# Kernel optimization log

Hardware: AMD Instinct MI355X
Metric: run time of the kernel (lower is better)

## Reference

```python
import jax, jax.numpy as jnp
import numpy as np

K = 3          # kernel size (3x3 branch of SConv_2d)
STRIDE = 1
PAD = 1
NONCENTER = jnp.array([0, 1, 2, 3, 5, 6, 7, 8])      # drop center (idx 4) before sort
REORDER = jnp.array([0, 1, 2, 3, 8, 4, 5, 6, 7])     # reinsert center in the middle


def setup_inputs() -> dict:
    key = jax.random.key(0)
    k1, k2, k3, k4 = jax.random.split(key, 4)
    B, Cin, H, Wd = 8, 64, 128, 128
    Cout = 128
    x = jax.random.normal(k1, (B, Cin, H, Wd), dtype=jnp.float32)
    Coefficient = jax.random.normal(k2, (K * K, K * K), dtype=jnp.float32)
    W = jax.random.normal(k3, (Cout, Cin, K, K), dtype=jnp.float32) * 0.05
    b = jax.random.normal(k4, (Cout,), dtype=jnp.float32) * 0.05
    return {"x": x, "Coefficient": Coefficient, "W": W, "b": b}


def reference(x, Coefficient, W, b):
    # pad (same=False -> constant padding PAD on all sides)
    xp = jnp.pad(x, ((0, 0), (0, 0), (PAD, PAD), (PAD, PAD)))
    B, C, Hp, Wp = xp.shape
    Ho = (Hp - K) // STRIDE + 1
    Wo = (Wp - K) // STRIDE + 1
    # unfold: patches[b, kh*K+kw, c, h, w] == torch unfold+view+permute layout [B, KH*KW, C, H*W]
    patches = jnp.stack(
        [xp[:, :, i:i + Ho * STRIDE:STRIDE, j:j + Wo * STRIDE:STRIDE]
         for i in range(K) for j in range(K)], axis=1)           # [B, 9, C, Ho, Wo]
    center = patches[:, 4:5]                                      # [B, 1, C, Ho, Wo]
    y = jnp.einsum('bjchw,ij->bichw', patches, Coefficient)       # [B, 9, C, Ho, Wo]
    ys = jnp.sort(y[:, NONCENTER], axis=1)                        # sort 8 non-center taps
    z = jnp.concatenate([ys, center], axis=1)                     # [B, 9, C, Ho, Wo]
    z = z[:, REORDER]
    # view(B, KH, KW, C, H, W).permute(0,3,4,1,5,2) -> [B, C, KH*H, KW*W]
    z = z.reshape(B, K, K, C, Ho, Wo).transpose(0, 3, 4, 1, 5, 2).reshape(B, C, K * Ho, K * Wo)
    out = jax.lax.conv_general_dilated(
        z, W, window_strides=(K, K), padding='VALID',
        dimension_numbers=('NCHW', 'OIHW', 'NCHW'))
    return out + b[None, :, None, None]
```

## Files before the change

kernel.cpp:

```cpp
#include <hip/hip_runtime.h>
#include <hip/hip_bf16.h>


#define B_   8
#define C_   64
#define H_   128
#define W_   128
#define CO_  128
#define K_   576
#define MT   64
#define SROW 584

typedef __attribute__((ext_vector_type(8)))  short  short8;
typedef __attribute__((ext_vector_type(8)))  __bf16 bf16x8;
typedef __attribute__((ext_vector_type(16))) float  f32x16;
typedef __attribute__((ext_vector_type(2)))  float  f32x2;

__device__ __forceinline__ void cswap2(f32x2 &a, f32x2 &b) {
    f32x2 lo = __builtin_elementwise_min(a, b);
    f32x2 hi = __builtin_elementwise_max(a, b);
    a = lo; b = hi;
}

__device__ __forceinline__ ushort f2bf(float f) {
    union { float f; unsigned u; } v; v.f = f;
    unsigned r = v.u + 0x7fffu + ((v.u >> 16) & 1u);
    return (ushort)(r >> 16);
}

__device__ __forceinline__ unsigned pack2bf(float lo, float hi) {
    union { __hip_bfloat162 h; unsigned u; } cv;
    cv.h = __float22bfloat162_rn(make_float2(lo, hi));
    return cv.u;
}

__global__ __launch_bounds__(256) void conv_W_bf16(const float* __restrict__ Wg,
                                                   ushort* __restrict__ Wb) {
    int i = blockIdx.x * 256 + threadIdx.x;
    if (i >= CO_ * K_) return;
    const int e    = i & 7;
    const int lane = (i >> 3) & 63;
    const int t9   = i >> 9;
    const int nt   = t9 / 36;
    const int ks   = t9 - nt * 36;
    const int co   = nt * 32 + (lane & 31);
    const int kp   = ks * 16 + (lane >> 5) * 8 + e;
    int c, t;
    if (kp < 512) { const int rc = kp >> 3; t = kp & 7; c = ((rc & 7) << 3) | (rc >> 3); }
    else          { c = kp - 512; t = 8; }
    Wb[i] = f2bf(Wg[co * K_ + c * 9 + t]);
}

__global__ __launch_bounds__(512, 4) void sconv_mfma(
    const float* __restrict__ x,
    const float* __restrict__ Coef,
    const ushort* __restrict__ Wb,
    const float* __restrict__ bias,
    float* __restrict__ out)
{
    __shared__ __align__(16) ushort Zl[MT * SROW];

    const int tid = threadIdx.x;
    const int bx  = blockIdx.x;
    const int wq  = bx & 7;
    const int hq  = (bx >> 3) & 31;
    const int b   = bx >> 8;
    const int w0  = wq * 16;
    const int h0  = hq * 4;

    const int wave = tid >> 6;
    const int lane = tid & 63;
    const int mt   = wave >> 2;
    const int nt   = wave & 3;
    const int r31  = lane & 31;
    const int u    = lane >> 5;
    const ushort* bptr = Wb + ((size_t)(nt * 36) * 64 + lane) * 8;

    {
        const int j  = (tid >> 3) & 7;
        const int c  = wave + 8 * j;
        const int pw = tid & 7;
        const int w  = w0 + pw * 2;
        const float* xb = x + ((size_t)(b * C_ + c)) * (H_ * W_);

        float r[6][4];
        const bool interior = (h0 >= 4) && (h0 <= 120) && (w0 >= 16) && (w0 <= 96);
        if (interior) {
            const float* bp = xb + (h0 - 1) * W_ + (w - 1);
            #pragma unroll
            for (int dy = 0; dy < 6; ++dy) {
                float4 v; __builtin_memcpy(&v, bp + dy * W_, 16);
                r[dy][0] = v.x; r[dy][1] = v.y; r[dy][2] = v.z; r[dy][3] = v.w;
            }
        } else {
            const int wm = w - 1;
            const int wc = min(max(wm, 0), W_ - 4);
            const int s  = wm - wc;
            #pragma unroll
            for (int dy = 0; dy < 6; ++dy) {
                const int hy  = h0 + dy - 1;
                const bool hok = (unsigned)hy < (unsigned)H_;
                const int hc  = min(max(hy, 0), H_ - 1);
                float4 v; __builtin_memcpy(&v, xb + hc * W_ + wc, 16);
                const float rr0 = (s < 0) ? 0.f : ((s > 0) ? v.y : v.x);
                const float rr1 = (s < 0) ? v.x : ((s > 0) ? v.z : v.y);
                const float rr2 = (s < 0) ? v.y : ((s > 0) ? v.w : v.z);
                const float rr3 = (s < 0) ? v.z : ((s > 0) ? 0.f : v.w);
                r[dy][0] = hok ? rr0 : 0.f;
                r[dy][1] = hok ? rr1 : 0.f;
                r[dy][2] = hok ? rr2 : 0.f;
                r[dy][3] = hok ? rr3 : 0.f;
            }
        }

        const int rcb  = (wave * 8 + j) << 4;
        const int tailb = 1024 + 2 * c;
        #pragma unroll
        for (int hl = 0; hl < 4; ++hl) {
            f32x2 p2[9];
            #pragma unroll
            for (int dy = 0; dy < 3; ++dy)
                #pragma unroll
                for (int dx = 0; dx < 3; ++dx)
                    p2[dy * 3 + dx] = (f32x2){ r[hl + dy][dx], r[hl + dy][dx + 1] };

            f32x2 v2[8];
            #pragma unroll
            for (int ii = 0; ii < 8; ++ii) {
                const int i = ii + (ii >> 2);
                f32x2 acc = p2[0] * Coef[i * 9];
                #pragma unroll
                for (int jj = 1; jj < 9; ++jj) acc += p2[jj] * Coef[i * 9 + jj];
                v2[ii] = acc;
            }

            cswap2(v2[0],v2[1]); cswap2(v2[2],v2[3]); cswap2(v2[4],v2[5]); cswap2(v2[6],v2[7]);
            cswap2(v2[0],v2[2]); cswap2(v2[1],v2[3]); cswap2(v2[4],v2[6]); cswap2(v2[5],v2[7]);
            cswap2(v2[1],v2[2]); cswap2(v2[5],v2[6]);
            cswap2(v2[0],v2[4]); cswap2(v2[1],v2[5]); cswap2(v2[2],v2[6]); cswap2(v2[3],v2[7]);
            cswap2(v2[2],v2[4]); cswap2(v2[3],v2[5]);
            cswap2(v2[1],v2[2]); cswap2(v2[3],v2[4]); cswap2(v2[5],v2[6]);

            f32x2 z2[9] = { v2[0], v2[1], v2[2], v2[3], p2[4],
                            v2[4], v2[5], v2[6], v2[7] };

            char* zb0 = (char*)Zl + (size_t)(hl * 16 + pw * 2) * (SROW * 2);
            char* zb1 = zb0 + SROW * 2;
            uint4 q0 = make_uint4(pack2bf(z2[0][0], z2[1][0]), pack2bf(z2[2][0], z2[3][0]),
                                  pack2bf(z2[4][0], z2[5][0]), pack2bf(z2[6][0], z2[7][0]));
            uint4 q1 = make_uint4(pack2bf(z2[0][1], z2[1][1]), pack2bf(z2[2][1], z2[3][1]),
                                  pack2bf(z2[4][1], z2[5][1]), pack2bf(z2[6][1], z2[7][1]));
            *(uint4*)(zb0 + rcb) = q0;
            *(uint4*)(zb1 + rcb) = q1;
            *(ushort*)(zb0 + tailb) = f2bf(z2[8][0]);
            *(ushort*)(zb1 + tailb) = f2bf(z2[8][1]);
        }
    }

    short8 bq[8];
    #pragma unroll
    for (int i = 0; i < 8; ++i) bq[i] = *(const short8*)(bptr + i * 512);

    __syncthreads();

    const int arow = mt * 32 + r31;
    const char* abase = (const char*)Zl + (size_t)arow * (SROW * 2) + u * 16;

    bf16x8 aq[4];
    #pragma unroll
    for (int i = 0; i < 4; ++i)
        aq[i] = *(const bf16x8*)(abase + i * 32);

    f32x16 acc = {};

    #pragma unroll
    for (int ks = 0; ks < 36; ++ks) {
        bf16x8 a  = aq[ks & 3];
        short8 bb = bq[ks & 7];
        if (ks + 4 < 36)
            aq[ks & 3] = *(const bf16x8*)(abase + (ks + 4) * 32);
        if (ks + 8 < 36)
            bq[ks & 7] = *(const short8*)(bptr + (ks + 8) * 512);
        acc = __builtin_amdgcn_mfma_f32_32x32x16_bf16(a, __builtin_bit_cast(bf16x8, bb), acc, 0, 0, 0);
    }

    const int co = nt * 32 + r31;
    const float bv = bias[co];
    float* obase = out + (((size_t)(b * CO_ + co)) * H_ + h0 + mt * 2) * W_ + w0;
    #pragma unroll
    for (int qq = 0; qq < 4; ++qq) {
        const int roff = qq * 8 + u * 4;
        const int hl   = roff >> 4;
        const int wl   = roff & 15;
        float4 vv = make_float4(acc[qq*4+0] + bv, acc[qq*4+1] + bv,
                                acc[qq*4+2] + bv, acc[qq*4+3] + bv);
        *(float4*)(obase + hl * W_ + wl) = vv;
    }
}

#define WT 16
__device__ __forceinline__ void cswap(float &a, float &b) {
    float lo = fminf(a, b);
    float hi = fmaxf(a, b);
    a = lo; b = hi;
}
__global__ __launch_bounds__(256) void sconv_fp32(
    const float* __restrict__ x, const float* __restrict__ Coef,
    const float* __restrict__ Wg, const float* __restrict__ bias,
    float* __restrict__ out)
{
    __shared__ float Cf[81];
    __shared__ float Zl[C_ * 9 * WT];
    const int tid = threadIdx.x;
    const int bx  = blockIdx.x;
    const int wt  = bx & 7;
    const int h   = (bx >> 3) & 127;
    const int b   = bx >> 10;
    const int w0  = wt * WT;
    if (tid < 81) Cf[tid] = Coef[tid];
    __syncthreads();
    for (int task = tid; task < C_ * WT; task += 256) {
        const int c = task >> 4, wl = task & 15, w = w0 + wl;
        const float* xb = x + (b * C_ + c) * H_ * W_;
        float p[9];
        #pragma unroll
        for (int dy = 0; dy < 3; ++dy) {
            const int hy = h + dy - 1; const bool hin = (unsigned)hy < (unsigned)H_;
            #pragma unroll
            for (int dx = 0; dx < 3; ++dx) {
                const int wx = w + dx - 1; const bool win = (unsigned)wx < (unsigned)W_;
                p[dy * 3 + dx] = (hin && win) ? xb[hy * W_ + wx] : 0.0f;
            }
        }
        float v[8];
        #pragma unroll
        for (int ii = 0; ii < 8; ++ii) {
            const int i = ii + (ii >> 2);
            float acc = 0.0f;
            #pragma unroll
            for (int j = 0; j < 9; ++j) acc = fmaf(Cf[i * 9 + j], p[j], acc);
            v[ii] = acc;
        }
        cswap(v[0], v[1]); cswap(v[2], v[3]); cswap(v[4], v[5]); cswap(v[6], v[7]);
        cswap(v[0], v[2]); cswap(v[1], v[3]); cswap(v[4], v[6]); cswap(v[5], v[7]);
        cswap(v[1], v[2]); cswap(v[5], v[6]);
        cswap(v[0], v[4]); cswap(v[1], v[5]); cswap(v[2], v[6]); cswap(v[3], v[7]);
        cswap(v[2], v[4]); cswap(v[3], v[5]);
        cswap(v[1], v[2]); cswap(v[3], v[4]); cswap(v[5], v[6]);
        const int base = c * 9 * WT + wl;
        Zl[base + 0*WT]=v[0]; Zl[base + 1*WT]=v[1]; Zl[base + 2*WT]=v[2]; Zl[base + 3*WT]=v[3];
        Zl[base + 4*WT]=p[4];
        Zl[base + 5*WT]=v[4]; Zl[base + 6*WT]=v[5]; Zl[base + 7*WT]=v[6]; Zl[base + 8*WT]=v[7];
    }
    __syncthreads();
    const int co = tid >> 1, w0l = (tid & 1) * 8;
    float acc[8];
    #pragma unroll
    for (int i = 0; i < 8; ++i) acc[i] = 0.0f;
    for (int c = 0; c < C_; ++c) {
        #pragma unroll
        for (int t = 0; t < 9; ++t) {
            const float wv = Wg[(co * C_ + c) * 9 + t];
            const float* zp = &Zl[(c * 9 + t) * WT + w0l];
            const float4 za = *(const float4*)zp;
            const float4 zb = *(const float4*)(zp + 4);
            acc[0]=fmaf(za.x,wv,acc[0]); acc[1]=fmaf(za.y,wv,acc[1]);
            acc[2]=fmaf(za.z,wv,acc[2]); acc[3]=fmaf(za.w,wv,acc[3]);
            acc[4]=fmaf(zb.x,wv,acc[4]); acc[5]=fmaf(zb.y,wv,acc[5]);
            acc[6]=fmaf(zb.z,wv,acc[6]); acc[7]=fmaf(zb.w,wv,acc[7]);
        }
    }
    const float bv = bias[co];
    float* op = out + ((b * CO_ + co) * H_ + h) * W_ + w0 + w0l;
    *(float4*)(op)     = make_float4(acc[0]+bv, acc[1]+bv, acc[2]+bv, acc[3]+bv);
    *(float4*)(op + 4) = make_float4(acc[4]+bv, acc[5]+bv, acc[6]+bv, acc[7]+bv);
}

extern "C" void kernel_launch(void* const* d_in, const int* in_sizes, int n_in,
                              void* d_out, int out_size, void* d_ws, size_t ws_size,
                              hipStream_t stream) {
    const float* x    = (const float*)d_in[0];
    const float* Coef = (const float*)d_in[1];
    const float* Wg   = (const float*)d_in[2];
    const float* bias = (const float*)d_in[3];
    float* out = (float*)d_out;

    const size_t need = (size_t)CO_ * K_ * sizeof(ushort);
    if (ws_size >= need) {
        ushort* Wb = (ushort*)d_ws;
        conv_W_bf16<<<(CO_ * K_ + 255) / 256, 256, 0, stream>>>(Wg, Wb);
        sconv_mfma<<<B_ * (H_ / 4) * (W_ / 16), 512, 0, stream>>>(x, Coef, Wb, bias, out);
    } else {
        sconv_fp32<<<B_ * H_ * 8, 256, 0, stream>>>(x, Coef, Wg, bias, out);
    }
}
```

Before: 143.7 us.

## Halve spatial tile and split K across waves with LDS reduction

Each block now covers 2 output rows instead of 4, which doubles the grid and halves the LDS tile. The 8 waves split the 36-step K loop into two halves of 18 per N-tile. The two partial accumulators are combined through LDS before the bias add and store. This aims to raise occupancy (launch bounds 4 to 6 blocks) and shorten each wave's MFMA chain. In exchange, the halo reload overhead per output row doubles, two extra barriers and an LDS reduction are added, and the same weights are reloaded by twice as many blocks.

Measured after the change: 135.8 us. 1.06x faster.

```diff
diff --git a/kernel.cpp b/kernel.cpp
--- a/kernel.cpp
+++ b/kernel.cpp
@@ -8,7 +8,7 @@
 #define W_   128
 #define CO_  128
 #define K_   576
-#define MT   64
+#define MT   32
 #define SROW 584
 
 typedef __attribute__((ext_vector_type(8)))  short  short8;
@@ -51,7 +51,7 @@
     Wb[i] = f2bf(Wg[co * K_ + c * 9 + t]);
 }
 
-__global__ __launch_bounds__(512, 4) void sconv_mfma(
+__global__ __launch_bounds__(512, 6) void sconv_mfma(
     const float* __restrict__ x,
     const float* __restrict__ Coef,
     const ushort* __restrict__ Wb,
@@ -63,18 +63,18 @@
     const int tid = threadIdx.x;
     const int bx  = blockIdx.x;
     const int wq  = bx & 7;
-    const int hq  = (bx >> 3) & 31;
-    const int b   = bx >> 8;
+    const int hp  = (bx >> 3) & 63;
+    const int b   = bx >> 9;
     const int w0  = wq * 16;
-    const int h0  = hq * 4;
+    const int h0  = hp * 2;
 
     const int wave = tid >> 6;
     const int lane = tid & 63;
-    const int mt   = wave >> 2;
     const int nt   = wave & 3;
+    const int kh   = wave >> 2;
     const int r31  = lane & 31;
     const int u    = lane >> 5;
-    const ushort* bptr = Wb + ((size_t)(nt * 36) * 64 + lane) * 8;
+    const ushort* bptr = Wb + ((size_t)(nt * 36 + kh * 18) * 64 + lane) * 8;
 
     {
         const int j  = (tid >> 3) & 7;
@@ -83,12 +83,12 @@
         const int w  = w0 + pw * 2;
         const float* xb = x + ((size_t)(b * C_ + c)) * (H_ * W_);
 
-        float r[6][4];
-        const bool interior = (h0 >= 4) && (h0 <= 120) && (w0 >= 16) && (w0 <= 96);
+        float r[4][4];
+        const bool interior = (h0 >= 2) && (h0 <= 124) && (w0 >= 16) && (w0 <= 96);
         if (interior) {
             const float* bp = xb + (h0 - 1) * W_ + (w - 1);
             #pragma unroll
-            for (int dy = 0; dy < 6; ++dy) {
+            for (int dy = 0; dy < 4; ++dy) {
                 float4 v; __builtin_memcpy(&v, bp + dy * W_, 16);
                 r[dy][0] = v.x; r[dy][1] = v.y; r[dy][2] = v.z; r[dy][3] = v.w;
             }
@@ -97,7 +97,7 @@
             const int wc = min(max(wm, 0), W_ - 4);
             const int s  = wm - wc;
             #pragma unroll
-            for (int dy = 0; dy < 6; ++dy) {
+            for (int dy = 0; dy < 4; ++dy) {
                 const int hy  = h0 + dy - 1;
                 const bool hok = (unsigned)hy < (unsigned)H_;
                 const int hc  = min(max(hy, 0), H_ - 1);
@@ -116,7 +116,7 @@
         const int rcb  = (wave * 8 + j) << 4;
         const int tailb = 1024 + 2 * c;
         #pragma unroll
-        for (int hl = 0; hl < 4; ++hl) {
+        for (int hl = 0; hl < 2; ++hl) {
             f32x2 p2[9];
             #pragma unroll
             for (int dy = 0; dy < 3; ++dy)
@@ -157,44 +157,63 @@
         }
     }
 
-    short8 bq[8];
+    short8 bq[4];
     #pragma unroll
-    for (int i = 0; i < 8; ++i) bq[i] = *(const short8*)(bptr + i * 512);
-
-    __syncthreads();
-
-    const int arow = mt * 32 + r31;
-    const char* abase = (const char*)Zl + (size_t)arow * (SROW * 2) + u * 16;
-
-    bf16x8 aq[4];
+    for (int i = 0; i < 4; ++i) bq[i] = *(const short8*)(bptr + i * 512);
+
+    __syncthreads();
+
+    const char* abase = (const char*)Zl + (size_t)r31 * (SROW * 2) + u * 16
+                        + kh * 18 * 32;
+
+    bf16x8 aq[2];
+    aq[0] = *(const bf16x8*)(abase + 0);
+    aq[1] = *(const bf16x8*)(abase + 32);
+
+    f32x16 acc = {};
+
     #pragma unroll
-    for (int i = 0; i < 4; ++i)
-        aq[i] = *(const bf16x8*)(abase + i * 32);
-
-    f32x16 acc = {};
-
-    #pragma unroll
-    for (int ks = 0; ks < 36; ++ks) {
-        bf16x8 a  = aq[ks & 3];
-        short8 bb = bq[ks & 7];
-        if (ks + 4 < 36)
-            aq[ks & 3] = *(const bf16x8*)(abase + (ks + 4) * 32);
-        if (ks + 8 < 36)
-            bq[ks & 7] = *(const short8*)(bptr + (ks + 8) * 512);
+    for (int ksl = 0; ksl < 18; ++ksl) {
+        bf16x8 a  = aq[ksl & 1];
+        short8 bb = bq[ksl & 3];
+        if (ksl + 2 < 18)
+            aq[ksl & 1] = *(const bf16x8*)(abase + (ksl + 2) * 32);
+        if (ksl + 4 < 18)
+            bq[ksl & 3] = *(const short8*)(bptr + (ksl + 4) * 512);
         acc = __builtin_amdgcn_mfma_f32_32x32x16_bf16(a, __builtin_bit_cast(bf16x8, bb), acc, 0, 0, 0);
     }
 
-    const int co = nt * 32 + r31;
-    const float bv = bias[co];
-    float* obase = out + (((size_t)(b * CO_ + co)) * H_ + h0 + mt * 2) * W_ + w0;
-    #pragma unroll
-    for (int qq = 0; qq < 4; ++qq) {
-        const int roff = qq * 8 + u * 4;
-        const int hl   = roff >> 4;
-        const int wl   = roff & 15;
-        float4 vv = make_float4(acc[qq*4+0] + bv, acc[qq*4+1] + bv,
-                                acc[qq*4+2] + bv, acc[qq*4+3] + bv);
-        *(float4*)(obase + hl * W_ + wl) = vv;
+    __syncthreads();
+    float* scratch = (float*)Zl;
+    if (kh == 1) {
+        float* sp = scratch + nt * 1088 + lane * 17;
+        #pragma unroll
+        for (int qq = 0; qq < 4; ++qq)
+            *(float4*)(sp + qq * 4) = make_float4(acc[qq*4+0], acc[qq*4+1],
+                                                  acc[qq*4+2], acc[qq*4+3]);
+    }
+    __syncthreads();
+    if (kh == 0) {
+        const float* sp = scratch + nt * 1088 + lane * 17;
+        #pragma unroll
+        for (int qq = 0; qq < 4; ++qq) {
+            float4 pv = *(const float4*)(sp + qq * 4);
+            acc[qq*4+0] += pv.x; acc[qq*4+1] += pv.y;
+            acc[qq*4+2] += pv.z; acc[qq*4+3] += pv.w;
+        }
+
+        const int co = nt * 32 + r31;
+        const float bv = bias[co];
+        float* obase = out + (((size_t)(b * CO_ + co)) * H_ + h0) * W_ + w0;
+        #pragma unroll
+        for (int qq = 0; qq < 4; ++qq) {
+            const int roff = qq * 8 + u * 4;
+            const int hl   = roff >> 4;
+            const int wl   = roff & 15;
+            float4 vv = make_float4(acc[qq*4+0] + bv, acc[qq*4+1] + bv,
+                                    acc[qq*4+2] + bv, acc[qq*4+3] + bv);
+            *(float4*)(obase + hl * W_ + wl) = vv;
+        }
     }
 }
 
@@ -289,7 +308,7 @@
     if (ws_size >= need) {
         ushort* Wb = (ushort*)d_ws;
         conv_W_bf16<<<(CO_ * K_ + 255) / 256, 256, 0, stream>>>(Wg, Wb);
-        sconv_mfma<<<B_ * (H_ / 4) * (W_ / 16), 512, 0, stream>>>(x, Coef, Wb, bias, out);
+        sconv_mfma<<<B_ * (H_ / 2) * (W_ / 16), 512, 0, stream>>>(x, Coef, Wb, bias, out);
     } else {
         sconv_fp32<<<B_ * H_ * 8, 256, 0, stream>>>(x, Coef, Wg, bias, out);
     }
```

## Double-buffer Z tiles and loop four row-pair steps per block, overlapping transform with MFMA

Applied to the files above, without the earlier changes.

Each block now covers 8 output rows in four steps of 2 rows, using a double-buffered LDS Z tile so that waves 4-7 build the next tile's sorted-tap transform while waves 0-3 run the MFMA GEMM on the current one. Input rows are carried between steps so each step loads only 2 new rows, cutting the halo reloads. The grid is halved and only half the waves issue MFMAs. Per-block work becomes more serial, and waves 0-3 take part in both the transform and the MFMA phases.

Result: no change. 144.8 us (+0.8%).

```diff
diff --git a/kernel.cpp b/kernel.cpp
--- a/kernel.cpp
+++ b/kernel.cpp
@@ -8,8 +8,9 @@
 #define W_   128
 #define CO_  128
 #define K_   576
-#define MT   64
+#define MT   32
 #define SROW 584
+#define TB   4
 
 typedef __attribute__((ext_vector_type(8)))  short  short8;
 typedef __attribute__((ext_vector_type(8)))  __bf16 bf16x8;
@@ -51,6 +52,72 @@
     Wb[i] = f2bf(Wg[co * K_ + c * 9 + t]);
 }
 
+__device__ __forceinline__ void load_row(const float* __restrict__ xb, int hy,
+                                         int w, bool wint, float out[4]) {
+    if (wint && (unsigned)hy < (unsigned)H_) {
+        float4 v; __builtin_memcpy(&v, xb + hy * W_ + (w - 1), 16);
+        out[0] = v.x; out[1] = v.y; out[2] = v.z; out[3] = v.w;
+    } else {
+        const bool hok = (unsigned)hy < (unsigned)H_;
+        const int hc = min(max(hy, 0), H_ - 1);
+        const int wm = w - 1;
+        const int wc = min(max(wm, 0), W_ - 4);
+        const int s  = wm - wc;
+        float4 v; __builtin_memcpy(&v, xb + hc * W_ + wc, 16);
+        const float r0 = (s < 0) ? 0.f : ((s > 0) ? v.y : v.x);
+        const float r1 = (s < 0) ? v.x : ((s > 0) ? v.z : v.y);
+        const float r2 = (s < 0) ? v.y : ((s > 0) ? v.w : v.z);
+        const float r3 = (s < 0) ? v.z : ((s > 0) ? 0.f : v.w);
+        out[0] = hok ? r0 : 0.f; out[1] = hok ? r1 : 0.f;
+        out[2] = hok ? r2 : 0.f; out[3] = hok ? r3 : 0.f;
+    }
+}
+
+__device__ __forceinline__ void zstore_tile(const float (&rr)[4][4],
+                                            const float* __restrict__ Coef,
+                                            char* bufb, int rcb, int tailb, int pw) {
+    #pragma unroll
+    for (int hl = 0; hl < 2; ++hl) {
+        f32x2 p2[9];
+        #pragma unroll
+        for (int dy = 0; dy < 3; ++dy)
+            #pragma unroll
+            for (int dx = 0; dx < 3; ++dx)
+                p2[dy * 3 + dx] = (f32x2){ rr[hl + dy][dx], rr[hl + dy][dx + 1] };
+
+        f32x2 v2[8];
+        #pragma unroll
+        for (int ii = 0; ii < 8; ++ii) {
+            const int i = ii + (ii >> 2);
+            f32x2 acc = p2[0] * Coef[i * 9];
+            #pragma unroll
+            for (int jj = 1; jj < 9; ++jj) acc += p2[jj] * Coef[i * 9 + jj];
+            v2[ii] = acc;
+        }
+
+        cswap2(v2[0],v2[1]); cswap2(v2[2],v2[3]); cswap2(v2[4],v2[5]); cswap2(v2[6],v2[7]);
+        cswap2(v2[0],v2[2]); cswap2(v2[1],v2[3]); cswap2(v2[4],v2[6]); cswap2(v2[5],v2[7]);
+        cswap2(v2[1],v2[2]); cswap2(v2[5],v2[6]);
+        cswap2(v2[0],v2[4]); cswap2(v2[1],v2[5]); cswap2(v2[2],v2[6]); cswap2(v2[3],v2[7]);
+        cswap2(v2[2],v2[4]); cswap2(v2[3],v2[5]);
+        cswap2(v2[1],v2[2]); cswap2(v2[3],v2[4]); cswap2(v2[5],v2[6]);
+
+        f32x2 z2[9] = { v2[0], v2[1], v2[2], v2[3], p2[4],
+                        v2[4], v2[5], v2[6], v2[7] };
+
+        char* zb0 = bufb + (size_t)(hl * 16 + pw * 2) * (SROW * 2);
+        char* zb1 = zb0 + SROW * 2;
+        uint4 q0 = make_uint4(pack2bf(z2[0][0], z2[1][0]), pack2bf(z2[2][0], z2[3][0]),
+                              pack2bf(z2[4][0], z2[5][0]), pack2bf(z2[6][0], z2[7][0]));
+        uint4 q1 = make_uint4(pack2bf(z2[0][1], z2[1][1]), pack2bf(z2[2][1], z2[3][1]),
+                              pack2bf(z2[4][1], z2[5][1]), pack2bf(z2[6][1], z2[7][1]));
+        *(uint4*)(zb0 + rcb) = q0;
+        *(uint4*)(zb1 + rcb) = q1;
+        *(ushort*)(zb0 + tailb) = f2bf(z2[8][0]);
+        *(ushort*)(zb1 + tailb) = f2bf(z2[8][1]);
+    }
+}
+
 __global__ __launch_bounds__(512, 4) void sconv_mfma(
     const float* __restrict__ x,
     const float* __restrict__ Coef,
@@ -58,143 +125,90 @@
     const float* __restrict__ bias,
     float* __restrict__ out)
 {
-    __shared__ __align__(16) ushort Zl[MT * SROW];
+    __shared__ __align__(16) ushort Zl[2][MT * SROW];
 
     const int tid = threadIdx.x;
     const int bx  = blockIdx.x;
     const int wq  = bx & 7;
-    const int hq  = (bx >> 3) & 31;
-    const int b   = bx >> 8;
+    const int hq  = (bx >> 3) & 15;
+    const int b   = bx >> 7;
     const int w0  = wq * 16;
-    const int h0  = hq * 4;
+    const int h0b = hq * 8;
 
     const int wave = tid >> 6;
     const int lane = tid & 63;
-    const int mt   = wave >> 2;
     const int nt   = wave & 3;
     const int r31  = lane & 31;
     const int u    = lane >> 5;
     const ushort* bptr = Wb + ((size_t)(nt * 36) * 64 + lane) * 8;
 
-    {
-        const int j  = (tid >> 3) & 7;
-        const int c  = wave + 8 * j;
-        const int pw = tid & 7;
-        const int w  = w0 + pw * 2;
-        const float* xb = x + ((size_t)(b * C_ + c)) * (H_ * W_);
-
-        float r[6][4];
-        const bool interior = (h0 >= 4) && (h0 <= 120) && (w0 >= 16) && (w0 <= 96);
-        if (interior) {
-            const float* bp = xb + (h0 - 1) * W_ + (w - 1);
-            #pragma unroll
-            for (int dy = 0; dy < 6; ++dy) {
-                float4 v; __builtin_memcpy(&v, bp + dy * W_, 16);
-                r[dy][0] = v.x; r[dy][1] = v.y; r[dy][2] = v.z; r[dy][3] = v.w;
+    const int j  = (tid >> 3) & 7;
+    const int c  = wave + 8 * j;
+    const int pw = tid & 7;
+    const int w  = w0 + pw * 2;
+    const float* xb = x + ((size_t)(b * C_ + c)) * (H_ * W_);
+    const bool wint = (w0 >= 16) && (w0 <= 96);
+    const int rcb   = (wave * 8 + j) << 4;
+    const int tailb = 1024 + 2 * c;
+
+    short8 bq[4];
+    if (wave < 4) {
+        #pragma unroll
+        for (int i = 0; i < 4; ++i) bq[i] = *(const short8*)(bptr + i * 512);
+    }
+
+    float rr[4][4];
+    load_row(xb, h0b - 1, w, wint, rr[0]);
+    load_row(xb, h0b + 0, w, wint, rr[1]);
+    load_row(xb, h0b + 1, w, wint, rr[2]);
+    load_row(xb, h0b + 2, w, wint, rr[3]);
+    zstore_tile(rr, Coef, (char*)&Zl[0][0], rcb, tailb, pw);
+    __syncthreads();
+
+    for (int t = 0; t < TB; ++t) {
+        if (t < TB - 1) {
+            #pragma unroll
+            for (int q2 = 0; q2 < 4; ++q2) { rr[0][q2] = rr[2][q2]; rr[1][q2] = rr[3][q2]; }
+            const int h0n = h0b + 2 * (t + 1);
+            load_row(xb, h0n + 1, w, wint, rr[2]);
+            load_row(xb, h0n + 2, w, wint, rr[3]);
+            zstore_tile(rr, Coef, (char*)&Zl[(t + 1) & 1][0], rcb, tailb, pw);
+        }
+        if (wave < 4) {
+            const char* abase = (const char*)&Zl[t & 1][0] + (size_t)r31 * (SROW * 2) + u * 16;
+            bf16x8 aq[2];
+            aq[0] = *(const bf16x8*)(abase + 0);
+            aq[1] = *(const bf16x8*)(abase + 32);
+            f32x16 acc = {};
+            #pragma unroll
+            for (int ks = 0; ks < 36; ++ks) {
+                bf16x8 a  = aq[ks & 1];
+                short8 bb = bq[ks & 3];
+                if (ks + 2 < 36)
+                    aq[ks & 1] = *(const bf16x8*)(abase + (ks + 2) * 32);
+                if (ks + 4 < 36)
+                    bq[ks & 3] = *(const short8*)(bptr + (ks + 4) * 512);
+                acc = __builtin_amdgcn_mfma_f32_32x32x16_bf16(a, __builtin_bit_cast(bf16x8, bb), acc, 0, 0, 0);
             }
-        } else {
-            const int wm = w - 1;
-            const int wc = min(max(wm, 0), W_ - 4);
-            const int s  = wm - wc;
-            #pragma unroll
-            for (int dy = 0; dy < 6; ++dy) {
-                const int hy  = h0 + dy - 1;
-                const bool hok = (unsigned)hy < (unsigned)H_;
-                const int hc  = min(max(hy, 0), H_ - 1);
-                float4 v; __builtin_memcpy(&v, xb + hc * W_ + wc, 16);
-                const float rr0 = (s < 0) ? 0.f : ((s > 0) ? v.y : v.x);
-                const float rr1 = (s < 0) ? v.x : ((s > 0) ? v.z : v.y);
-                const float rr2 = (s < 0) ? v.y : ((s > 0) ? v.w : v.z);
-                const float rr3 = (s < 0) ? v.z : ((s > 0) ? 0.f : v.w);
-                r[dy][0] = hok ? rr0 : 0.f;
-                r[dy][1] = hok ? rr1 : 0.f;
-                r[dy][2] = hok ? rr2 : 0.f;
-                r[dy][3] = hok ? rr3 : 0.f;
+            if (t < TB - 1) {
+                #pragma unroll
+                for (int i = 0; i < 4; ++i) bq[i] = *(const short8*)(bptr + i * 512);
             }
-        }
-
-        const int rcb  = (wave * 8 + j) << 4;
-        const int tailb = 1024 + 2 * c;
-        #pragma unroll
-        for (int hl = 0; hl < 4; ++hl) {
-            f32x2 p2[9];
-            #pragma unroll
-            for (int dy = 0; dy < 3; ++dy)
-                #pragma unroll
-                for (int dx = 0; dx < 3; ++dx)
-                    p2[dy * 3 + dx] = (f32x2){ r[hl + dy][dx], r[hl + dy][dx + 1] };
-
-            f32x2 v2[8];
-            #pragma unroll
-            for (int ii = 0; ii < 8; ++ii) {
-                const int i = ii + (ii >> 2);
-                f32x2 acc = p2[0] * Coef[i * 9];
-                #pragma unroll
-                for (int jj = 1; jj < 9; ++jj) acc += p2[jj] * Coef[i * 9 + jj];
-                v2[ii] = acc;
+            const int h0t = h0b + 2 * t;
+            const int co  = nt * 32 + r31;
+            const float bv = bias[co];
+            float* obase = out + (((size_t)(b * CO_ + co)) * H_ + h0t) * W_ + w0;
+            #pragma unroll
+            for (int qq = 0; qq < 4; ++qq) {
+                const int roff = qq * 8 + u * 4;
+                const int hl   = roff >> 4;
+                const int wl   = roff & 15;
+                *(float4*)(obase + hl * W_ + wl) =
+                    make_float4(acc[qq*4+0] + bv, acc[qq*4+1] + bv,
+                                acc[qq*4+2] + bv, acc[qq*4+3] + bv);
             }
-
-            cswap2(v2[0],v2[1]); cswap2(v2[2],v2[3]); cswap2(v2[4],v2[5]); cswap2(v2[6],v2[7]);
-            cswap2(v2[0],v2[2]); cswap2(v2[1],v2[3]); cswap2(v2[4],v2[6]); cswap2(v2[5],v2[7]);
-            cswap2(v2[1],v2[2]); cswap2(v2[5],v2[6]);
-            cswap2(v2[0],v2[4]); cswap2(v2[1],v2[5]); cswap2(v2[2],v2[6]); cswap2(v2[3],v2[7]);
-            cswap2(v2[2],v2[4]); cswap2(v2[3],v2[5]);
-            cswap2(v2[1],v2[2]); cswap2(v2[3],v2[4]); cswap2(v2[5],v2[6]);
-
-            f32x2 z2[9] = { v2[0], v2[1], v2[2], v2[3], p2[4],
-                            v2[4], v2[5], v2[6], v2[7] };
-
-            char* zb0 = (char*)Zl + (size_t)(hl * 16 + pw * 2) * (SROW * 2);
-            char* zb1 = zb0 + SROW * 2;
-            uint4 q0 = make_uint4(pack2bf(z2[0][0], z2[1][0]), pack2bf(z2[2][0], z2[3][0]),
-                                  pack2bf(z2[4][0], z2[5][0]), pack2bf(z2[6][0], z2[7][0]));
-            uint4 q1 = make_uint4(pack2bf(z2[0][1], z2[1][1]), pack2bf(z2[2][1], z2[3][1]),
-                                  pack2bf(z2[4][1], z2[5][1]), pack2bf(z2[6][1], z2[7][1]));
-            *(uint4*)(zb0 + rcb) = q0;
-            *(uint4*)(zb1 + rcb) = q1;
-            *(ushort*)(zb0 + tailb) = f2bf(z2[8][0]);
-            *(ushort*)(zb1 + tailb) = f2bf(z2[8][1]);
-        }
-    }
-
-    short8 bq[8];
-    #pragma unroll
-    for (int i = 0; i < 8; ++i) bq[i] = *(const short8*)(bptr + i * 512);
-
-    __syncthreads();
-
-    const int arow = mt * 32 + r31;
-    const char* abase = (const char*)Zl + (size_t)arow * (SROW * 2) + u * 16;
-
-    bf16x8 aq[4];
-    #pragma unroll
-    for (int i = 0; i < 4; ++i)
-        aq[i] = *(const bf16x8*)(abase + i * 32);
-
-    f32x16 acc = {};
-
-    #pragma unroll
-    for (int ks = 0; ks < 36; ++ks) {
-        bf16x8 a  = aq[ks & 3];
-        short8 bb = bq[ks & 7];
-        if (ks + 4 < 36)
-            aq[ks & 3] = *(const bf16x8*)(abase + (ks + 4) * 32);
-        if (ks + 8 < 36)
-            bq[ks & 7] = *(const short8*)(bptr + (ks + 8) * 512);
-        acc = __builtin_amdgcn_mfma_f32_32x32x16_bf16(a, __builtin_bit_cast(bf16x8, bb), acc, 0, 0, 0);
-    }
-
-    const int co = nt * 32 + r31;
-    const float bv = bias[co];
-    float* obase = out + (((size_t)(b * CO_ + co)) * H_ + h0 + mt * 2) * W_ + w0;
-    #pragma unroll
-    for (int qq = 0; qq < 4; ++qq) {
-        const int roff = qq * 8 + u * 4;
-        const int hl   = roff >> 4;
-        const int wl   = roff & 15;
-        float4 vv = make_float4(acc[qq*4+0] + bv, acc[qq*4+1] + bv,
-                                acc[qq*4+2] + bv, acc[qq*4+3] + bv);
-        *(float4*)(obase + hl * W_ + wl) = vv;
+        }
+        __syncthreads();
     }
 }
 
@@ -238,7 +252,7 @@
             const int i = ii + (ii >> 2);
             float acc = 0.0f;
             #pragma unroll
-            for (int j = 0; j < 9; ++j) acc = fmaf(Cf[i * 9 + j], p[j], acc);
+            for (int jj = 0; jj < 9; ++jj) acc = fmaf(Cf[i * 9 + jj], p[jj], acc);
             v[ii] = acc;
         }
         cswap(v[0], v[1]); cswap(v[2], v[3]); cswap(v[4], v[5]); cswap(v[6], v[7]);
@@ -289,7 +303,7 @@
     if (ws_size >= need) {
         ushort* Wb = (ushort*)d_ws;
         conv_W_bf16<<<(CO_ * K_ + 255) / 256, 256, 0, stream>>>(Wg, Wb);
-        sconv_mfma<<<B_ * (H_ / 4) * (W_ / 16), 512, 0, stream>>>(x, Coef, Wb, bias, out);
+        sconv_mfma<<<B_ * (H_ / 8) * (W_ / 16), 512, 0, stream>>>(x, Coef, Wb, bias, out);
     } else {
         sconv_fp32<<<B_ * H_ * 8, 256, 0, stream>>>(x, Coef, Wg, bias, out);
     }
```
